# Kernel tuning notes

Measured on AMD Instinct MI355X. Metric: run time of the kernel, lower is better.

The kernel has to match this reference:

```python
import jax, jax.numpy as jnp
import numpy as np

C = 256          # channels
NUM_HEADS = 4
HEAD_DIM = C // NUM_HEADS
TILE_SIZE = 64
TILE_SEQ = TILE_SIZE * TILE_SIZE  # 4096
B, H_IMG, W_IMG = 1, 96, 96
EPS = 1e-5


def setup_inputs() -> dict:
    key = jax.random.key(0)
    k0, k1, k2 = jax.random.split(key, 3)
    x = jax.random.normal(k0, (B, C, H_IMG, W_IMG), jnp.float32)
    norm_w = jnp.ones((C,), jnp.float32)
    norm_b = jnp.zeros((C,), jnp.float32)
    qkv_w = jax.random.normal(k1, (3 * C, C), jnp.float32) * (C ** -0.5)
    qkv_b = jnp.zeros((3 * C,), jnp.float32)
    proj_w = jax.random.normal(k2, (C, C), jnp.float32) * (C ** -0.5)
    proj_b = jnp.zeros((C,), jnp.float32)
    return {"x": x, "norm_w": norm_w, "norm_b": norm_b,
            "qkv_w": qkv_w, "qkv_b": qkv_b,
            "proj_w": proj_w, "proj_b": proj_b}


def _attn(q, k, v, scale):
    # q: [B,H,Q,D], k/v: [B,H,K,D]
    s = jnp.einsum('bhqd,bhkd->bhqk', q, k) * scale
    p = jax.nn.softmax(s, axis=-1)
    return jnp.einsum('bhqk,bhkd->bhqd', p, v)


def reference(x, norm_w, norm_b, qkv_w, qkv_b, proj_w, proj_b):
    b, c, h, w = x.shape
    seq = h * w
    g = min(32, c)
    # GroupNorm
    xg = x.reshape(b, g, c // g, h, w)
    mean = xg.mean(axis=(2, 3, 4), keepdims=True)
    var = ((xg - mean) ** 2).mean(axis=(2, 3, 4), keepdims=True)
    xn = (xg - mean) * jax.lax.rsqrt(var + EPS)
    xn = xn.reshape(b, c, h, w) * norm_w[None, :, None, None] + norm_b[None, :, None, None]
    # flatten spatial -> tokens
    xf = xn.transpose(0, 2, 3, 1).reshape(b, seq, c)
    qkv = xf @ qkv_w.T + qkv_b  # [B,S,3C]
    qkv = qkv.reshape(b, seq, 3, NUM_HEADS, HEAD_DIM).transpose(2, 0, 3, 1, 4)
    q, k, v = qkv[0], qkv[1], qkv[2]  # [B,H,S,D]
    scale = HEAD_DIM ** -0.5
    if seq > TILE_SEQ:
        num_tiles = (seq + TILE_SEQ - 1) // TILE_SEQ
        outs = []
        for i in range(num_tiles):  # small fixed tile count, static slices
            s0 = i * TILE_SEQ
            e0 = min((i + 1) * TILE_SEQ, seq)
            k0 = max(0, s0 - TILE_SEQ // 2)
            k1 = min(seq, e0 + TILE_SEQ // 2)
            outs.append(_attn(q[:, :, s0:e0], k[:, :, k0:k1], v[:, :, k0:k1], scale))
        out = jnp.concatenate(outs, axis=2)
    else:
        out = _attn(q, k, v, scale)
    out = out.transpose(0, 2, 1, 3).reshape(b, seq, c)
    out = out @ proj_w.T + proj_b
    out = out.reshape(b, h, w, c).transpose(0, 3, 1, 2)
    return out + x
```

## Files before the change

### kernel.cpp

```cpp
#include <hip/hip_runtime.h>

typedef __bf16 bf16x8 __attribute__((ext_vector_type(8)));
typedef float f32x4 __attribute__((ext_vector_type(4)));
typedef float f32x16 __attribute__((ext_vector_type(16)));
typedef int i32x4 __attribute__((ext_vector_type(4)));
typedef int i32x2 __attribute__((ext_vector_type(2)));
typedef unsigned short u16x4 __attribute__((ext_vector_type(4)));

#define S_TOK 9216
#define LOG2E 1.44269504088896340736f
#define SCALE_Q (0.125f * LOG2E)

__device__ inline unsigned short f2bf(float f) {
    unsigned int u = __builtin_bit_cast(unsigned int, f);
    return (unsigned short)((u + 0x7fffu + ((u >> 16) & 1u)) >> 16);
}

__device__ inline unsigned int cvt_pk_bf16(float lo, float hi) {
    unsigned int r;
    asm("v_cvt_pk_bf16_f32 %0, %1, %2" : "=v"(r) : "v"(lo), "v"(hi));
    return r;
}

__device__ inline void permswap(unsigned int& a, unsigned int& b) {
    asm("v_permlane32_swap_b32 %0, %1" : "+v"(a), "+v"(b));
}

__device__ inline f32x4 MFMA(bf16x8 a, bf16x8 b, f32x4 c) {
    return __builtin_amdgcn_mfma_f32_16x16x32_bf16(a, b, c, 0, 0, 0);
}
__device__ inline f32x16 MFMA32(bf16x8 a, bf16x8 b, f32x16 c) {
    return __builtin_amdgcn_mfma_f32_32x32x16_bf16(a, b, c, 0, 0, 0);
}

__device__ inline int swz(int row, int c) {
    return ((c + (row >> 3)) & 7) ^ (row & 7);
}
__device__ inline bf16x8 load_frag(const unsigned short* lds, int outer, int kbase) {
    int lane = threadIdx.x & 63;
    int row = outer + (lane & 15);
    int cc = swz(row, (kbase >> 3) + (lane >> 4));
    return *reinterpret_cast<const bf16x8*>(lds + row * 64 + cc * 8);
}
__device__ inline bf16x8 load_frag32(const unsigned short* lds, int outer, int kbase) {
    int lane = threadIdx.x & 63;
    int row = outer + (lane & 31);
    int cc = swz(row, (kbase >> 3) + (lane >> 5));
    return *reinterpret_cast<const bf16x8*>(lds + row * 64 + cc * 8);
}
__device__ inline void stage_tile(unsigned short* lds, const unsigned short* src,
                                  int stride, int nrows) {
    for (int id = threadIdx.x; id < nrows * 8; id += 256) {
        int row = id >> 3, cc = id & 7;
        i32x4 v = *reinterpret_cast<const i32x4*>(src + row * stride + cc * 8);
        *reinterpret_cast<i32x4*>(lds + row * 64 + swz(row, cc) * 8) = v;
    }
}

__global__ __launch_bounds__(256) void gn_stats_part(const float* __restrict__ x,
                                                     float* __restrict__ part) {
    int c = blockIdx.x;
    const f32x4* p = reinterpret_cast<const f32x4*>(x + c * S_TOK);
    float s = 0.f, ss = 0.f;
    for (int i = threadIdx.x; i < 2304; i += 256) {
        f32x4 v = p[i];
        s += v[0] + v[1] + v[2] + v[3];
        ss += v[0] * v[0] + v[1] * v[1] + v[2] * v[2] + v[3] * v[3];
    }
#pragma unroll
    for (int off = 1; off < 64; off <<= 1) {
        s += __shfl_xor(s, off);
        ss += __shfl_xor(ss, off);
    }
    __shared__ float rs[4], rss[4];
    int wave = threadIdx.x >> 6;
    if ((threadIdx.x & 63) == 0) { rs[wave] = s; rss[wave] = ss; }
    __syncthreads();
    if (threadIdx.x == 0) {
        part[c] = rs[0] + rs[1] + rs[2] + rs[3];
        part[256 + c] = rss[0] + rss[1] + rss[2] + rss[3];
    }
}

__global__ __launch_bounds__(256) void gn_apply(const float* __restrict__ x,
                                                const float* __restrict__ part,
                                                const float* __restrict__ nw,
                                                const float* __restrict__ nb,
                                                unsigned short* __restrict__ xf) {
    __shared__ float tl[64][65];
    __shared__ float gmean[8], grstd[8];
    int sb = blockIdx.x * 64, cb = blockIdx.y * 64;
    if (threadIdx.x < 8) {
        int g = (cb >> 3) + threadIdx.x;
        float s = 0.f, ss = 0.f;
#pragma unroll
        for (int i = 0; i < 8; ++i) { s += part[g * 8 + i]; ss += part[256 + g * 8 + i]; }
        float mean = s * (1.f / 73728.f);
        float var = ss * (1.f / 73728.f) - mean * mean;
        gmean[threadIdx.x] = mean;
        grstd[threadIdx.x] = rsqrtf(var + 1e-5f);
    }
    __syncthreads();
    for (int id = threadIdx.x; id < 1024; id += 256) {
        int cr = id >> 4;
        int sq = (id & 15) << 2;
        int c = cb + cr;
        f32x4 v = *reinterpret_cast<const f32x4*>(x + c * S_TOK + sb + sq);
        float mu = gmean[cr >> 3], rstd = grstd[cr >> 3];
        float wv = nw[c] * rstd;
        float bv = nb[c] - mu * wv;
#pragma unroll
        for (int j = 0; j < 4; ++j) tl[sq + j][cr] = v[j] * wv + bv;
    }
    __syncthreads();
    for (int id = threadIdx.x; id < 1024; id += 256) {
        int sr = id >> 4;
        int cq = (id & 15) << 2;
        u16x4 o;
#pragma unroll
        for (int j = 0; j < 4; ++j) o[j] = f2bf(tl[sr][cq + j]);
        *reinterpret_cast<u16x4*>(xf + (sb + sr) * 256 + cb + cq) = o;
    }
}

__global__ __launch_bounds__(256) void conv_bf16(const float* __restrict__ in,
                                                 unsigned short* __restrict__ out,
                                                 int n, int scaled_rows) {
    int i = blockIdx.x * 256 + threadIdx.x;
    if (i < n) {
        float sc = ((i >> 8) < scaled_rows) ? SCALE_Q : 1.0f;
        out[i] = f2bf(in[i] * sc);
    }
}

template <int MODE>
__global__ __launch_bounds__(256) void gemm_bt(const unsigned short* __restrict__ A,
                                               const unsigned short* __restrict__ B,
                                               const float* __restrict__ bias,
                                               unsigned short* __restrict__ q_out,
                                               unsigned short* __restrict__ k_out,
                                               unsigned short* __restrict__ vT_out,
                                               const float* __restrict__ xres,
                                               float* __restrict__ out) {
    __shared__ alignas(16) unsigned short As[128 * 64];
    __shared__ alignas(16) unsigned short Bs[128 * 64];
    int mb = blockIdx.x, nb = blockIdx.y;
    int wave = threadIdx.x >> 6, lane = threadIdx.x & 63;
    int wm = wave >> 1, wn = wave & 1;
    f32x4 zero = {0.f, 0.f, 0.f, 0.f};
    f32x4 acc[4][4];
    for (int i = 0; i < 4; ++i)
        for (int j = 0; j < 4; ++j) acc[i][j] = zero;
    for (int ks = 0; ks < 4; ++ks) {
        __syncthreads();
        stage_tile(As, A + (mb * 128) * 256 + ks * 64, 256, 128);
        stage_tile(Bs, B + (nb * 128) * 256 + ks * 64, 256, 128);
        __syncthreads();
#pragma unroll
        for (int kk = 0; kk < 2; ++kk) {
            bf16x8 af[4], bfr[4];
#pragma unroll
            for (int mt = 0; mt < 4; ++mt) af[mt] = load_frag(As, wm * 64 + mt * 16, kk * 32);
#pragma unroll
            for (int nt = 0; nt < 4; ++nt) bfr[nt] = load_frag(Bs, wn * 64 + nt * 16, kk * 32);
#pragma unroll
            for (int mt = 0; mt < 4; ++mt)
#pragma unroll
                for (int nt = 0; nt < 4; ++nt)
                    acc[mt][nt] = MFMA(af[mt], bfr[nt], acc[mt][nt]);
        }
    }
    int r0 = (lane >> 4) << 2;
    int cl = lane & 15;
#pragma unroll
    for (int mt = 0; mt < 4; ++mt) {
#pragma unroll
        for (int nt = 0; nt < 4; ++nt) {
            int m = mb * 128 + wm * 64 + mt * 16 + r0;
            int n = nb * 128 + wn * 64 + nt * 16 + cl;
            if (MODE == 0) {
                float bv = bias[n] * ((n < 256) ? SCALE_Q : 1.0f);
#pragma unroll
                for (int r = 0; r < 4; ++r) {
                    unsigned short hh = f2bf(acc[mt][nt][r] + bv);
                    int s = m + r;
                    if (n < 256) q_out[s * 256 + n] = hh;
                    else if (n < 512) k_out[s * 256 + (n - 256)] = hh;
                    else vT_out[(n - 512) * S_TOK + s] = hh;
                }
            } else {
                float bv = bias[n];
                f32x4 xr = *reinterpret_cast<const f32x4*>(xres + n * S_TOK + m);
                f32x4 o;
#pragma unroll
                for (int r = 0; r < 4; ++r) o[r] = acc[mt][nt][r] + bv + xr[r];
                *reinterpret_cast<f32x4*>(out + n * S_TOK + m) = o;
            }
        }
    }
}

struct StageRegs { i32x4 k0, k1, v0, v1; };

__device__ inline StageRegs load_stage(const unsigned short* ksrc, const unsigned short* vsrc) {
    int tid = threadIdx.x;
    int row = tid >> 3, cc = tid & 7;
    StageRegs r;
    r.k0 = *reinterpret_cast<const i32x4*>(ksrc + row * 256 + cc * 8);
    r.k1 = *reinterpret_cast<const i32x4*>(ksrc + (row + 32) * 256 + cc * 8);
    r.v0 = *reinterpret_cast<const i32x4*>(vsrc + row * S_TOK + cc * 8);
    r.v1 = *reinterpret_cast<const i32x4*>(vsrc + (row + 32) * S_TOK + cc * 8);
    return r;
}

__device__ inline void store_stage(unsigned short* K, unsigned short* V, StageRegs r) {
    int tid = threadIdx.x;
    int row = tid >> 3, cc = tid & 7;
    *reinterpret_cast<i32x4*>(K + row * 64 + swz(row, cc) * 8) = r.k0;
    *reinterpret_cast<i32x4*>(K + (row + 32) * 64 + swz(row + 32, cc) * 8) = r.k1;
    *reinterpret_cast<i32x4*>(V + row * 64 + swz(row, cc) * 8) = r.v0;
    *reinterpret_cast<i32x4*>(V + (row + 32) * 64 + swz(row + 32, cc) * 8) = r.v1;
}

template <int NC>
__global__ __launch_bounds__(256) void attn(const unsigned short* __restrict__ qb,
                                            const unsigned short* __restrict__ kb,
                                            const unsigned short* __restrict__ vT,
                                            unsigned short* __restrict__ Opart,
                                            float* __restrict__ lpart) {
    __shared__ alignas(16) unsigned short Ks[2][64 * 64];
    __shared__ alignas(16) unsigned short Vs[2][64 * 64];
    constexpr int NS0 = 96 / NC, NS1 = 112 / NC, NS2 = 48 / NC;
    constexpr int B0 = 32 * NS0, B1 = B0 + 32 * NS1, NB = B1 + 8 * NS2;

    int bx = blockIdx.x;
    int head = bx / NB;
    int r = bx % NB;
    int tile, seg, qi;
    if (r < B0)      { tile = 0; seg = r >> 5; qi = r & 31; }
    else if (r < B1) { int t = r - B0; tile = 1; seg = t >> 5; qi = t & 31; }
    else             { int t = r - B1; tile = 2; seg = t >> 3; qi = t & 7; }
    int qs0 = (tile == 0) ? 0 : (tile == 1 ? 4096 : 8192);
    int kv0 = (tile == 0) ? 0 : (tile == 1 ? 2048 : 6144);
    int qstart = qs0 + qi * 128;
    int c0 = seg * NC, c1 = c0 + NC;
    int wave = threadIdx.x >> 6, lane = threadIdx.x & 63;
    int l31 = lane & 31, h = lane >> 5;

    stage_tile((unsigned short*)Ks, qb + qstart * 256 + head * 64, 256, 128);
    __syncthreads();
    bf16x8 qf[4];
#pragma unroll
    for (int s = 0; s < 4; ++s) qf[s] = load_frag32((unsigned short*)Ks, wave * 32, s * 16);
    __syncthreads();

    bf16x8 ones;
#pragma unroll
    for (int i = 0; i < 8; ++i) ones[i] = (__bf16)1.0f;

    f32x16 oacc0, oacc1, lac;
#pragma unroll
    for (int i = 0; i < 16; ++i) { oacc0[i] = 0.f; oacc1[i] = 0.f; lac[i] = 0.f; }

    const unsigned short* kbase = kb + kv0 * 256 + head * 64;
    const unsigned short* vbase = vT + head * 64 * S_TOK + kv0;

    StageRegs R = load_stage(kbase + c0 * (64 * 256), vbase + c0 * 64);
    store_stage(Ks[c0 & 1], Vs[c0 & 1], R);
    if (c0 + 1 < c1) R = load_stage(kbase + (c0 + 1) * (64 * 256), vbase + (c0 + 1) * 64);
    __syncthreads();

    for (int ch = c0; ch < c1; ++ch) {
        int p = ch & 1;
        if (ch + 1 < c1) {
            store_stage(Ks[p ^ 1], Vs[p ^ 1], R);
            if (ch + 2 < c1)
                R = load_stage(kbase + (ch + 2) * (64 * 256), vbase + (ch + 2) * 64);
        }
        const unsigned short* Kp = Ks[p];
        const unsigned short* Vp = Vs[p];
        f32x16 sc0, sc1;
#pragma unroll
        for (int i = 0; i < 16; ++i) { sc0[i] = 0.f; sc1[i] = 0.f; }
        __builtin_amdgcn_s_setprio(1);
#pragma unroll
        for (int s = 0; s < 4; ++s) {
            bf16x8 k0 = load_frag32(Kp, 0, s * 16);
            bf16x8 k1 = load_frag32(Kp, 32, s * 16);
            sc0 = MFMA32(k0, qf[s], sc0);
            sc1 = MFMA32(k1, qf[s], sc1);
        }
#pragma unroll
        for (int s = 0; s < 4; ++s) {
            f32x16 scr = (s < 2) ? sc0 : sc1;
            const int b = 8 * (s & 1);
            float E[8];
#pragma unroll
            for (int i = 0; i < 8; ++i) E[i] = __builtin_amdgcn_exp2f(scr[b + i]);
            unsigned int p01 = cvt_pk_bf16(E[0], E[1]);
            unsigned int p23 = cvt_pk_bf16(E[2], E[3]);
            unsigned int p45 = cvt_pk_bf16(E[4], E[5]);
            unsigned int p67 = cvt_pk_bf16(E[6], E[7]);
            unsigned int u = h ? p01 : p45;
            unsigned int v = h ? p23 : p67;
            permswap(u, v);
            permswap(v, u);
            i32x4 w;
            w[0] = (int)(h ? v : p01);
            w[1] = (int)(h ? u : p23);
            w[2] = (int)(h ? p45 : v);
            w[3] = (int)(h ? p67 : u);
            bf16x8 pa = __builtin_bit_cast(bf16x8, w);
            bf16x8 v0 = load_frag32(Vp, 0, s * 16);
            bf16x8 v1 = load_frag32(Vp, 32, s * 16);
            oacc0 = MFMA32(pa, v0, oacc0);
            oacc1 = MFMA32(pa, v1, oacc1);
            lac = MFMA32(pa, ones, lac);
        }
        __builtin_amdgcn_s_setprio(0);
        __syncthreads();
    }
    unsigned int obase = (unsigned int)seg * (S_TOK * 256);
#pragma unroll
    for (int reg = 0; reg < 16; ++reg) {
        int qloc = (reg & 3) + 8 * (reg >> 2) + 4 * h;
        int s = qstart + wave * 32 + qloc;
        Opart[obase + s * 256 + head * 64 + l31] =
            __builtin_bit_cast(unsigned short, (__bf16)oacc0[reg]);
        Opart[obase + s * 256 + head * 64 + 32 + l31] =
            __builtin_bit_cast(unsigned short, (__bf16)oacc1[reg]);
    }
    if (l31 == 0) {
#pragma unroll
        for (int reg = 0; reg < 16; ++reg) {
            int qloc = (reg & 3) + 8 * (reg >> 2) + 4 * h;
            int s = qstart + wave * 32 + qloc;
            lpart[(seg * 4 + head) * S_TOK + s] = lac[reg];
        }
    }
}

template <int NC>
__global__ __launch_bounds__(256) void combine(const unsigned short* __restrict__ Op,
                                               const float* __restrict__ lp,
                                               unsigned short* __restrict__ att) {
    int idx = blockIdx.x * 256 + threadIdx.x;
    int s = idx >> 5;
    int c0 = (idx & 31) << 3;
    int head = c0 >> 6;
    int nseg = (s < 4096) ? (96 / NC) : (s < 8192 ? (112 / NC) : (48 / NC));
    float acc[8] = {0.f, 0.f, 0.f, 0.f, 0.f, 0.f, 0.f, 0.f};
    float l = 0.f;
    for (int seg = 0; seg < nseg; ++seg) {
        i32x4 v = *reinterpret_cast<const i32x4*>(Op + (size_t)seg * (S_TOK * 256) + s * 256 + c0);
        const unsigned short* u = reinterpret_cast<const unsigned short*>(&v);
#pragma unroll
        for (int i = 0; i < 8; ++i)
            acc[i] += __builtin_bit_cast(float, ((unsigned int)u[i]) << 16);
        l += lp[(seg * 4 + head) * S_TOK + s];
    }
    float inv = 1.f / l;
    u16x4 o0, o1;
#pragma unroll
    for (int i = 0; i < 4; ++i) {
        o0[i] = f2bf(acc[i] * inv);
        o1[i] = f2bf(acc[4 + i] * inv);
    }
    unsigned short* dst = att + s * 256 + c0;
    *reinterpret_cast<u16x4*>(dst) = o0;
    *reinterpret_cast<u16x4*>(dst + 4) = o1;
}

extern "C" void kernel_launch(void* const* d_in, const int* in_sizes, int n_in,
                              void* d_out, int out_size, void* d_ws, size_t ws_size,
                              hipStream_t stream) {
    const float* x      = (const float*)d_in[0];
    const float* norm_w = (const float*)d_in[1];
    const float* norm_b = (const float*)d_in[2];
    const float* qkv_w  = (const float*)d_in[3];
    const float* qkv_b  = (const float*)d_in[4];
    const float* proj_w = (const float*)d_in[5];
    const float* proj_b = (const float*)d_in[6];
    float* outp = (float*)d_out;

    char* wsb = (char*)d_ws;
    float* part = (float*)wsb;
    unsigned short* xf    = (unsigned short*)(wsb + 2048);
    unsigned short* qkvw  = xf + 9216 * 256;
    unsigned short* projw = qkvw + 768 * 256;
    unsigned short* qbuf  = projw + 256 * 256;
    unsigned short* kbuf  = qbuf + 9216 * 256;
    unsigned short* vTbuf = kbuf + 9216 * 256;
    unsigned short* Opart = vTbuf + 256 * 9216;
    size_t fixed_bytes = 2048 + 2ull * 256 * (9216ull * 4 + 768 + 256);
    size_t need8 = fixed_bytes + 2ull * 14 * 9216 * 256 + 4ull * 14 * 4 * 9216;
    bool use8 = (ws_size >= need8);
    int MS = use8 ? 14 : 7;
    float* lpart = (float*)(Opart + (size_t)MS * 9216 * 256);
    unsigned short* attb  = xf;

    gn_stats_part<<<dim3(256), dim3(256), 0, stream>>>(x, part);
    gn_apply<<<dim3(144, 4), dim3(256), 0, stream>>>(x, part, norm_w, norm_b, xf);
    conv_bf16<<<dim3(768), dim3(256), 0, stream>>>(qkv_w, qkvw, 768 * 256, 256);
    conv_bf16<<<dim3(256), dim3(256), 0, stream>>>(proj_w, projw, 256 * 256, 0);
    gemm_bt<0><<<dim3(72, 6), dim3(256), 0, stream>>>(xf, qkvw, qkv_b,
                                                      qbuf, kbuf, vTbuf, nullptr, nullptr);
    if (use8) {
        attn<8><<<dim3(4 * 880), dim3(256), 0, stream>>>(qbuf, kbuf, vTbuf, Opart, lpart);
        combine<8><<<dim3(1152), dim3(256), 0, stream>>>(Opart, lpart, attb);
    } else {
        attn<16><<<dim3(4 * 440), dim3(256), 0, stream>>>(qbuf, kbuf, vTbuf, Opart, lpart);
        combine<16><<<dim3(1152), dim3(256), 0, stream>>>(Opart, lpart, attb);
    }
    gemm_bt<1><<<dim3(72, 2), dim3(256), 0, stream>>>(attb, projw, proj_b,
                                                      nullptr, nullptr, nullptr, x, outp);
}
```

Before: 164.7 us.

## Merge weight conversion launches and simplify softmax P-fragment lane permutation

```diff
diff --git a/kernel.cpp b/kernel.cpp
--- a/kernel.cpp
+++ b/kernel.cpp
@@ -123,14 +123,14 @@
     }
 }
 
-__global__ __launch_bounds__(256) void conv_bf16(const float* __restrict__ in,
-                                                 unsigned short* __restrict__ out,
-                                                 int n, int scaled_rows) {
+__global__ __launch_bounds__(256) void conv_both(const float* __restrict__ qkvw_in,
+                                                 const float* __restrict__ projw_in,
+                                                 unsigned short* __restrict__ out) {
     int i = blockIdx.x * 256 + threadIdx.x;
-    if (i < n) {
-        float sc = ((i >> 8) < scaled_rows) ? SCALE_Q : 1.0f;
-        out[i] = f2bf(in[i] * sc);
-    }
+    float v;
+    if (i < 768 * 256) v = qkvw_in[i] * ((i < 256 * 256) ? SCALE_Q : 1.0f);
+    else v = projw_in[i - 768 * 256];
+    out[i] = f2bf(v);
 }
 
 template <int MODE>
@@ -296,20 +296,15 @@
             const int b = 8 * (s & 1);
             float E[8];
 #pragma unroll
-            for (int i = 0; i < 8; ++i) E[i] = __builtin_amdgcn_exp2f(scr[b + i]);
-            unsigned int p01 = cvt_pk_bf16(E[0], E[1]);
-            unsigned int p23 = cvt_pk_bf16(E[2], E[3]);
-            unsigned int p45 = cvt_pk_bf16(E[4], E[5]);
-            unsigned int p67 = cvt_pk_bf16(E[6], E[7]);
-            unsigned int u = h ? p01 : p45;
-            unsigned int v = h ? p23 : p67;
-            permswap(u, v);
-            permswap(v, u);
+            for (int i = 0; i < 8; ++i) E[i] = exp2f(scr[b + i]);
+            unsigned int w0 = cvt_pk_bf16(E[0], E[1]);
+            unsigned int w1 = cvt_pk_bf16(E[2], E[3]);
+            unsigned int w2 = cvt_pk_bf16(E[4], E[5]);
+            unsigned int w3 = cvt_pk_bf16(E[6], E[7]);
+            permswap(w0, w2);
+            permswap(w1, w3);
             i32x4 w;
-            w[0] = (int)(h ? v : p01);
-            w[1] = (int)(h ? u : p23);
-            w[2] = (int)(h ? p45 : v);
-            w[3] = (int)(h ? p67 : u);
+            w[0] = (int)w0; w[1] = (int)w1; w[2] = (int)w2; w[3] = (int)w3;
             bf16x8 pa = __builtin_bit_cast(bf16x8, w);
             bf16x8 v0 = load_frag32(Vp, 0, s * 16);
             bf16x8 v1 = load_frag32(Vp, 32, s * 16);
@@ -401,8 +396,7 @@
 
     gn_stats_part<<<dim3(256), dim3(256), 0, stream>>>(x, part);
     gn_apply<<<dim3(144, 4), dim3(256), 0, stream>>>(x, part, norm_w, norm_b, xf);
-    conv_bf16<<<dim3(768), dim3(256), 0, stream>>>(qkv_w, qkvw, 768 * 256, 256);
-    conv_bf16<<<dim3(256), dim3(256), 0, stream>>>(proj_w, projw, 256 * 256, 0);
+    conv_both<<<dim3(1024), dim3(256), 0, stream>>>(qkv_w, proj_w, qkvw);
     gemm_bt<0><<<dim3(72, 6), dim3(256), 0, stream>>>(xf, qkvw, qkv_b,
                                                       qbuf, kbuf, vTbuf, nullptr, nullptr);
     if (use8) {
```

Result: slower. 178.6 us (+8.4%).
